# Optimization experiments

Measured on AMD Instinct MI355X. Metric: run time of the kernel, lower is better.

Reference implementation:

```python
import jax, jax.numpy as jnp
import numpy as np

N0, N1, N2 = 819200, 81920, 8192
E1, E2 = 819200, 81920
DIN, DH, DOUT = 128, 256, 128


def setup_inputs() -> dict:
    key = jax.random.key(0)
    ks = jax.random.split(key, 12)
    inp = {
        "x": jax.random.normal(ks[0], (N0, DIN), dtype=jnp.float32),
        "src1": jax.random.randint(ks[1], (E1,), 0, N0, dtype=jnp.int32),
        "dst1": jax.random.randint(ks[2], (E1,), 0, N1, dtype=jnp.int32),
        "src2": jax.random.randint(ks[3], (E2,), 0, N1, dtype=jnp.int32),
        "dst2": jax.random.randint(ks[4], (E2,), 0, N2, dtype=jnp.int32),
        "n1": N1,
        "n2": N2,
        # SAGEConv layer 1 params (lin_l has bias, lin_r no bias, PyG default)
        "w1l": jax.random.normal(ks[5], (DIN, DH), dtype=jnp.float32) / np.sqrt(DIN),
        "b1": jnp.zeros((DH,), dtype=jnp.float32),
        "w1r": jax.random.normal(ks[6], (DIN, DH), dtype=jnp.float32) / np.sqrt(DIN),
        # SAGEConv layer 2 params
        "w2l": jax.random.normal(ks[7], (DH, DOUT), dtype=jnp.float32) / np.sqrt(DH),
        "b2": jnp.zeros((DOUT,), dtype=jnp.float32),
        "w2r": jax.random.normal(ks[8], (DH, DOUT), dtype=jnp.float32) / np.sqrt(DH),
    }
    return inp


def _sage_conv(x_src, x_dst, src, dst, n_dst, wl, bl, wr):
    # mean aggregation of neighbor (source) features into destinations
    msg = x_src[src]                                            # [E, d]
    agg = jax.ops.segment_sum(msg, dst, num_segments=n_dst)     # [n_dst, d]
    cnt = jax.ops.segment_sum(jnp.ones((dst.shape[0],), msg.dtype), dst,
                              num_segments=n_dst)               # [n_dst]
    mean = agg / jnp.maximum(cnt, 1.0)[:, None]
    return mean @ wl + bl + x_dst @ wr


def reference(x, src1, dst1, src2, dst2, n1, n2, w1l, b1, w1r, w2l, b2, w2r):
    # layer 1 (eval mode: dropout is a no-op)
    h = _sage_conv(x, x[:n1], src1, dst1, n1, w1l, b1, w1r)     # [n1, DH]
    h = jax.nn.relu(h)
    # layer 2
    out = _sage_conv(h, h[:n2], src2, dst2, n2, w2l, b2, w2r)   # [n2, DOUT]
    return out
```

## Files before the change

kernel.cpp:

```cpp
#include <hip/hip_runtime.h>

constexpr int cN0 = 819200, cN1 = 81920, cN2 = 8192;
constexpr int cE1 = 819200, cE2 = 81920;
constexpr int cDIN = 128, cDH = 256, cDOUT = 128;
constexpr int cNOFF = cN1 + cN2;

typedef __attribute__((ext_vector_type(8))) short bf16x8;
typedef __attribute__((ext_vector_type(4))) float f32x4;
typedef __attribute__((ext_vector_type(8))) unsigned short u16x8;

__device__ __forceinline__ unsigned short f2bf(float f) {
    unsigned u = __builtin_bit_cast(unsigned, f);
    u += 0x7FFF + ((u >> 16) & 1);
    return (unsigned short)(u >> 16);
}
__device__ __forceinline__ float bf2f(unsigned short s) {
    unsigned u = ((unsigned)s) << 16;
    return __builtin_bit_cast(float, u);
}

#define GLOAD_LDS16(g, l) __builtin_amdgcn_global_load_lds(               \
    (const __attribute__((address_space(1))) void*)(g),                   \
    (__attribute__((address_space(3))) void*)(l), 16, 0, 0)

__global__ __launch_bounds__(256) void setup_k(
    int* __restrict__ offs,
    const float* __restrict__ w1l, const float* __restrict__ w1r,
    const float* __restrict__ w2l, const float* __restrict__ w2r,
    unsigned short* __restrict__ W1c, unsigned short* __restrict__ W2c,
    const float* __restrict__ x, unsigned short* __restrict__ xb)
{
    int id = blockIdx.x * 256 + threadIdx.x;
    if (id < cNOFF) { offs[id] = 0; return; }
    id -= cNOFF;
    if (id < 256 * 256) {
        int n = id >> 8, k = id & 255;
        float v = (k < 128) ? w1l[k * 256 + n] : w1r[(k - 128) * 256 + n];
        W1c[n * 256 + k] = f2bf(v);
        return;
    }
    id -= 256 * 256;
    if (id < 128 * 512) {
        int n = id >> 9, k = id & 511;
        float v = (k < 256) ? w2l[k * 128 + n] : w2r[(k - 256) * 128 + n];
        W2c[n * 512 + k] = f2bf(v);
        return;
    }
    id -= 128 * 512;
    {
        const float* p = x + (size_t)id * 8;
        float4 a = *reinterpret_cast<const float4*>(p);
        float4 b = *reinterpret_cast<const float4*>(p + 4);
        u16x8 o;
        o[0] = f2bf(a.x); o[1] = f2bf(a.y); o[2] = f2bf(a.z); o[3] = f2bf(a.w);
        o[4] = f2bf(b.x); o[5] = f2bf(b.y); o[6] = f2bf(b.z); o[7] = f2bf(b.w);
        reinterpret_cast<u16x8*>(xb)[id] = o;
    }
}

__global__ __launch_bounds__(256) void hist_k(
    const int* __restrict__ dst1, const int* __restrict__ dst2,
    int* __restrict__ offs)
{
    int e = blockIdx.x * 256 + threadIdx.x;
    if (e < cE1) atomicAdd(&offs[dst1[e]], 1);
    else {
        int e2 = e - cE1;
        if (e2 < cE2) atomicAdd(&offs[cN1 + dst2[e2]], 1);
    }
}

__global__ __launch_bounds__(1024) void partial_k(
    const int* __restrict__ a, int* __restrict__ part)
{
    const int tid = threadIdx.x, lane = tid & 63, wid = tid >> 6;
    int v = a[blockIdx.x * 1024 + tid];
    #pragma unroll
    for (int off = 32; off; off >>= 1) v += __shfl_xor(v, off);
    __shared__ int ws[16];
    if (lane == 0) ws[wid] = v;
    __syncthreads();
    if (tid == 0) {
        int s = 0;
        #pragma unroll
        for (int i = 0; i < 16; ++i) s += ws[i];
        part[blockIdx.x] = s;
    }
}

__global__ __launch_bounds__(128) void scanp_k(int* __restrict__ part)
{
    const int tid = threadIdx.x, lane = tid & 63, wid = tid >> 6;
    int v = (tid < 88) ? part[tid] : 0;
    int incl = v;
    #pragma unroll
    for (int off = 1; off < 64; off <<= 1) {
        int t = __shfl_up(incl, off, 64);
        if (lane >= off) incl += t;
    }
    __shared__ int w0;
    if (wid == 0 && lane == 63) w0 = incl;
    __syncthreads();
    int pre = wid ? w0 : 0;
    if (tid < 88) part[tid] = pre + incl - v;
}

__global__ __launch_bounds__(1024) void final_k(
    int* __restrict__ a, const int* __restrict__ part)
{
    const int tid = threadIdx.x, lane = tid & 63, wid = tid >> 6;
    const int g = blockIdx.x * 1024 + tid;
    int v = a[g];
    int incl = v;
    #pragma unroll
    for (int off = 1; off < 64; off <<= 1) {
        int t = __shfl_up(incl, off, 64);
        if (lane >= off) incl += t;
    }
    __shared__ int ws[16];
    if (lane == 63) ws[wid] = incl;
    __syncthreads();
    int pre = 0;
    #pragma unroll
    for (int i = 0; i < 16; ++i) if (i < wid) pre += ws[i];
    int r = part[blockIdx.x] + pre + incl - v;
    if (g >= cN1) r -= cE1;
    a[g] = r;
}

__global__ __launch_bounds__(256) void build_k(
    const int* __restrict__ src1, const int* __restrict__ dst1,
    const int* __restrict__ src2, const int* __restrict__ dst2,
    int* __restrict__ offs, int* __restrict__ eidx1, int* __restrict__ eidx2)
{
    int e = blockIdx.x * 256 + threadIdx.x;
    if (e < cE1) {
        int p = atomicAdd(&offs[dst1[e]], 1);
        eidx1[p] = src1[e];
    } else {
        int e2 = e - cE1;
        if (e2 < cE2) {
            int p = atomicAdd(&offs[cN1 + dst2[e2]], 1);
            eidx2[p] = src2[e2];
        }
    }
}

__global__ __launch_bounds__(256) void agg1_k(
    const float* __restrict__ x, const int* __restrict__ cursor,
    const int* __restrict__ eidx, unsigned short* __restrict__ mean1)
{
    const int row = blockIdx.x * 4 + (threadIdx.x >> 6);
    const int lane = threadIdx.x & 63;
    const int g = lane >> 4, li = lane & 15;
    const int start = row ? cursor[row - 1] : 0;
    const int end = cursor[row];
    float acc[8] = {};
    for (int e = start + g; e < end; e += 4) {
        const int s = eidx[e];
        const float4* p = reinterpret_cast<const float4*>(x + (size_t)s * cDIN + li * 8);
        float4 a = p[0], b = p[1];
        acc[0] += a.x; acc[1] += a.y; acc[2] += a.z; acc[3] += a.w;
        acc[4] += b.x; acc[5] += b.y; acc[6] += b.z; acc[7] += b.w;
    }
    #pragma unroll
    for (int i = 0; i < 8; ++i) {
        acc[i] += __shfl_xor(acc[i], 16);
        acc[i] += __shfl_xor(acc[i], 32);
    }
    if (g == 0) {
        const float inv = 1.0f / fmaxf((float)(end - start), 1.0f);
        u16x8 o;
        #pragma unroll
        for (int i = 0; i < 8; ++i) o[i] = f2bf(acc[i] * inv);
        *reinterpret_cast<u16x8*>(mean1 + (size_t)row * cDIN + li * 8) = o;
    }
}

__global__ __launch_bounds__(256) void agg2_k(
    const unsigned short* __restrict__ h, const int* __restrict__ cursor,
    const int* __restrict__ eidx, unsigned short* __restrict__ mean2)
{
    const int row = blockIdx.x * 4 + (threadIdx.x >> 6);
    const int lane = threadIdx.x & 63;
    const int g = lane >> 4, li = lane & 15;
    const int start = row ? cursor[row - 1] : 0;
    const int end = cursor[row];
    float acc[16] = {};
    for (int e = start + g; e < end; e += 4) {
        const int s = eidx[e];
        const u16x8* p = reinterpret_cast<const u16x8*>(h + (size_t)s * cDH + li * 16);
        u16x8 a = p[0], b = p[1];
        #pragma unroll
        for (int i = 0; i < 8; ++i) { acc[i] += bf2f(a[i]); acc[8 + i] += bf2f(b[i]); }
    }
    #pragma unroll
    for (int i = 0; i < 16; ++i) {
        acc[i] += __shfl_xor(acc[i], 16);
        acc[i] += __shfl_xor(acc[i], 32);
    }
    if (g == 0) {
        const float inv = 1.0f / fmaxf((float)(end - start), 1.0f);
        u16x8 o0, o1;
        #pragma unroll
        for (int i = 0; i < 8; ++i) { o0[i] = f2bf(acc[i] * inv); o1[i] = f2bf(acc[8 + i] * inv); }
        u16x8* q = reinterpret_cast<u16x8*>(mean2 + (size_t)row * cDH + li * 16);
        q[0] = o0; q[1] = o1;
    }
}

__global__ __launch_bounds__(256) void gemm1_k(
    const unsigned short* __restrict__ mean1,
    const unsigned short* __restrict__ xb,
    const unsigned short* __restrict__ W1c,
    const float* __restrict__ b1,
    unsigned short* __restrict__ h)
{
    __shared__ unsigned short As[128 * 32];
    __shared__ unsigned short Bs[128 * 32];

    const int tid = threadIdx.x;
    const int l = tid & 63, w = tid >> 6;
    const int q = l >> 4, r16 = l & 15;
    const int wr0 = (w >> 1) * 64, wc0 = (w & 1) * 64;
    const int n0 = blockIdx.x * 128, row0 = blockIdx.y * 128;

    const int srow = w * 32 + (l >> 2);
    const int skoff = (l & 3) * 8;

    const f32x4 zero = {0.f, 0.f, 0.f, 0.f};
    f32x4 acc[4][4];
    #pragma unroll
    for (int m = 0; m < 4; ++m)
        #pragma unroll
        for (int n = 0; n < 4; ++n) acc[m][n] = zero;

    for (int k0 = 0; k0 < 256; k0 += 32) {
        const unsigned short* Asrc = (k0 < 128) ? mean1 : xb;
        const int kk = k0 & 127;
        __syncthreads();
        #pragma unroll
        for (int j = 0; j < 2; ++j) {
            const int r = srow + j * 16;
            GLOAD_LDS16(Asrc + (size_t)(row0 + r) * 128 + kk + skoff,
                        As + (w * 2 + j) * 512);
            GLOAD_LDS16(W1c + (size_t)(n0 + r) * 256 + k0 + skoff,
                        Bs + (w * 2 + j) * 512);
        }
        __syncthreads();
        bf16x8 af[4], bg[4];
        #pragma unroll
        for (int m = 0; m < 4; ++m)
            af[m] = *reinterpret_cast<const bf16x8*>(As + (wr0 + 16 * m + r16) * 32 + q * 8);
        #pragma unroll
        for (int n = 0; n < 4; ++n)
            bg[n] = *reinterpret_cast<const bf16x8*>(Bs + (wc0 + 16 * n + r16) * 32 + q * 8);
        #pragma unroll
        for (int m = 0; m < 4; ++m)
            #pragma unroll
            for (int n = 0; n < 4; ++n)
                acc[m][n] = __builtin_amdgcn_mfma_f32_16x16x32_bf16(af[m], bg[n], acc[m][n], 0, 0, 0);
    }

    #pragma unroll
    for (int n = 0; n < 4; ++n) {
        const int col = n0 + wc0 + 16 * n + r16;
        const float bv = b1[col];
        #pragma unroll
        for (int m = 0; m < 4; ++m) {
            #pragma unroll
            for (int j = 0; j < 4; ++j) {
                const int row = row0 + wr0 + 16 * m + 4 * q + j;
                h[(size_t)row * cDH + col] = f2bf(fmaxf(acc[m][n][j] + bv, 0.f));
            }
        }
    }
}

__global__ __launch_bounds__(256) void gemm2_k(
    const unsigned short* __restrict__ mean2,
    const unsigned short* __restrict__ hd,
    const unsigned short* __restrict__ W2c,
    const float* __restrict__ b2, float* __restrict__ out)
{
    constexpr int K = 512, KL = 256, N = 128, TM = 64;
    constexpr int LD = 40;
    __shared__ unsigned short As[TM * LD];
    __shared__ unsigned short Bs[128 * LD];

    const int tid = threadIdx.x;
    const int l = tid & 63, w = tid >> 6;
    const int q = l >> 4, r16 = l & 15;
    const int wc0 = w * 32;
    const int row0 = blockIdx.y * TM;

    const f32x4 zero = {0.f, 0.f, 0.f, 0.f};
    f32x4 acc[4][2];
    #pragma unroll
    for (int m = 0; m < 4; ++m) { acc[m][0] = zero; acc[m][1] = zero; }

    for (int k0 = 0; k0 < K; k0 += 32) {
        const bool left = (k0 < KL);
        const unsigned short* Asrc = left ? mean2 : hd;
        const int kk = k0 & (KL - 1);
        __syncthreads();
        {
            int r = tid >> 2, o16 = tid & 3;
            bf16x8 av = *reinterpret_cast<const bf16x8*>(Asrc + (size_t)(row0 + r) * KL + kk + o16 * 8);
            *reinterpret_cast<bf16x8*>(As + r * LD + o16 * 8) = av;
        }
        #pragma unroll
        for (int c = 0; c < 2; ++c) {
            int z = tid + c * 256;
            int r = z >> 2, o16 = z & 3;
            bf16x8 bv = *reinterpret_cast<const bf16x8*>(W2c + (size_t)r * K + k0 + o16 * 8);
            *reinterpret_cast<bf16x8*>(Bs + r * LD + o16 * 8) = bv;
        }
        __syncthreads();
        bf16x8 af[4], bg[2];
        #pragma unroll
        for (int m = 0; m < 4; ++m)
            af[m] = *reinterpret_cast<const bf16x8*>(As + (16 * m + r16) * LD + q * 8);
        #pragma unroll
        for (int n = 0; n < 2; ++n)
            bg[n] = *reinterpret_cast<const bf16x8*>(Bs + (wc0 + 16 * n + r16) * LD + q * 8);
        #pragma unroll
        for (int m = 0; m < 4; ++m)
            #pragma unroll
            for (int n = 0; n < 2; ++n)
                acc[m][n] = __builtin_amdgcn_mfma_f32_16x16x32_bf16(af[m], bg[n], acc[m][n], 0, 0, 0);
    }

    #pragma unroll
    for (int n = 0; n < 2; ++n) {
        const int col = wc0 + 16 * n + r16;
        const float bv = b2[col];
        #pragma unroll
        for (int m = 0; m < 4; ++m) {
            #pragma unroll
            for (int j = 0; j < 4; ++j) {
                const int row = row0 + 16 * m + 4 * q + j;
                out[(size_t)row * N + col] = acc[m][n][j] + bv;
            }
        }
    }
}

extern "C" void kernel_launch(void* const* d_in, const int* in_sizes, int n_in,
                              void* d_out, int out_size, void* d_ws, size_t ws_size,
                              hipStream_t stream)
{
    const float* x    = (const float*)d_in[0];
    const int*   src1 = (const int*)d_in[1];
    const int*   dst1 = (const int*)d_in[2];
    const int*   src2 = (const int*)d_in[3];
    const int*   dst2 = (const int*)d_in[4];
    const float* w1l  = (const float*)d_in[7];
    const float* b1   = (const float*)d_in[8];
    const float* w1r  = (const float*)d_in[9];
    const float* w2l  = (const float*)d_in[10];
    const float* b2   = (const float*)d_in[11];
    const float* w2r  = (const float*)d_in[12];
    float* out = (float*)d_out;

    unsigned short* mean1 = (unsigned short*)d_ws;
    unsigned short* h     = mean1 + (size_t)cN1 * cDIN;
    unsigned short* mean2 = h + (size_t)cN1 * cDH;
    unsigned short* W1c   = mean2 + (size_t)cN2 * cDH;
    unsigned short* W2c   = W1c + 256 * 256;
    unsigned short* xb    = W2c + 128 * 512;
    int* offs  = (int*)(xb + (size_t)cN1 * cDIN);
    int* eidx1 = offs + cNOFF;
    int* eidx2 = eidx1 + cE1;
    int* part  = eidx2 + cE2;

    {
        int total = cNOFF + 256 * 256 + 128 * 512 + cN1 * cDIN / 8;
        setup_k<<<total / 256, 256, 0, stream>>>(offs, w1l, w1r, w2l, w2r,
                                                 W1c, W2c, x, xb);
    }
    hist_k<<<(cE1 + cE2) / 256, 256, 0, stream>>>(dst1, dst2, offs);
    partial_k<<<cNOFF / 1024, 1024, 0, stream>>>(offs, part);
    scanp_k<<<1, 128, 0, stream>>>(part);
    final_k<<<cNOFF / 1024, 1024, 0, stream>>>(offs, part);
    build_k<<<(cE1 + cE2) / 256, 256, 0, stream>>>(src1, dst1, src2, dst2, offs, eidx1, eidx2);

    agg1_k<<<cN1 / 4, 256, 0, stream>>>(x, offs, eidx1, mean1);
    gemm1_k<<<dim3(2, cN1 / 128), 256, 0, stream>>>(mean1, xb, W1c, b1, h);
    agg2_k<<<cN2 / 4, 256, 0, stream>>>(h, offs + cN1, eidx2, mean2);
    gemm2_k<<<dim3(1, cN2 / 64), 256, 0, stream>>>(mean2, h, W2c, b2, out);
}
```

Baseline: 246.1 us.

## Fuse histogram into setup, single-pass scan, and halve gemm2 row tile

Counter zeroing moves to a memset, and the destination histogram is folded into the setup kernel. The three-kernel scan (partial, scan of partials, final) becomes one kernel: block 0 spins on per-block flags to compute block prefixes and publishes them back. Together these cut the launch count and the dependency bubbles between the tiny preprocessing kernels. gemm2 uses 32-row tiles to double its block count for more parallelism on the small output, but each block now reloads the full weight matrix for half as many rows. The scan depends on all 88 blocks being co-resident, which holds on this GPU but is not guaranteed by the language.

```diff
diff --git a/kernel.cpp b/kernel.cpp
--- a/kernel.cpp
+++ b/kernel.cpp
@@ -2,8 +2,10 @@
 
 constexpr int cN0 = 819200, cN1 = 81920, cN2 = 8192;
 constexpr int cE1 = 819200, cE2 = 81920;
+constexpr int cEtot = cE1 + cE2;
 constexpr int cDIN = 128, cDH = 256, cDOUT = 128;
 constexpr int cNOFF = cN1 + cN2;
+constexpr int cSBLK = 88;
 
 typedef __attribute__((ext_vector_type(8))) short bf16x8;
 typedef __attribute__((ext_vector_type(4))) float f32x4;
@@ -23,16 +25,21 @@
     (const __attribute__((address_space(1))) void*)(g),                   \
     (__attribute__((address_space(3))) void*)(l), 16, 0, 0)
 
-__global__ __launch_bounds__(256) void setup_k(
+__global__ __launch_bounds__(256) void setup2_k(
     int* __restrict__ offs,
+    const int* __restrict__ dst1, const int* __restrict__ dst2,
     const float* __restrict__ w1l, const float* __restrict__ w1r,
     const float* __restrict__ w2l, const float* __restrict__ w2r,
     unsigned short* __restrict__ W1c, unsigned short* __restrict__ W2c,
     const float* __restrict__ x, unsigned short* __restrict__ xb)
 {
     int id = blockIdx.x * 256 + threadIdx.x;
-    if (id < cNOFF) { offs[id] = 0; return; }
-    id -= cNOFF;
+    if (id < cEtot) {
+        if (id < cE1) atomicAdd(&offs[dst1[id]], 1);
+        else atomicAdd(&offs[cN1 + dst2[id - cE1]], 1);
+        return;
+    }
+    id -= cEtot;
     if (id < 256 * 256) {
         int n = id >> 8, k = id & 255;
         float v = (k < 128) ? w1l[k * 256 + n] : w1r[(k - 128) * 256 + n];
@@ -58,72 +65,68 @@
     }
 }
 
-__global__ __launch_bounds__(256) void hist_k(
-    const int* __restrict__ dst1, const int* __restrict__ dst2,
-    int* __restrict__ offs)
-{
-    int e = blockIdx.x * 256 + threadIdx.x;
-    if (e < cE1) atomicAdd(&offs[dst1[e]], 1);
-    else {
-        int e2 = e - cE1;
-        if (e2 < cE2) atomicAdd(&offs[cN1 + dst2[e2]], 1);
-    }
-}
-
-__global__ __launch_bounds__(1024) void partial_k(
-    const int* __restrict__ a, int* __restrict__ part)
-{
-    const int tid = threadIdx.x, lane = tid & 63, wid = tid >> 6;
-    int v = a[blockIdx.x * 1024 + tid];
-    #pragma unroll
-    for (int off = 32; off; off >>= 1) v += __shfl_xor(v, off);
+__global__ __launch_bounds__(1024) void scan_lb_k(
+    int* __restrict__ a, unsigned* __restrict__ word)
+{
+    const int tid = threadIdx.x, bid = blockIdx.x;
+    const int lane = tid & 63, wid = tid >> 6;
+    const int g = bid * 1024 + tid;
     __shared__ int ws[16];
-    if (lane == 0) ws[wid] = v;
-    __syncthreads();
-    if (tid == 0) {
-        int s = 0;
-        #pragma unroll
-        for (int i = 0; i < 16; ++i) s += ws[i];
-        part[blockIdx.x] = s;
-    }
-}
-
-__global__ __launch_bounds__(128) void scanp_k(int* __restrict__ part)
-{
-    const int tid = threadIdx.x, lane = tid & 63, wid = tid >> 6;
-    int v = (tid < 88) ? part[tid] : 0;
+    __shared__ int aggs[cSBLK];
+    __shared__ int pex[cSBLK];
+    __shared__ int sh_excl;
+
+    int v = a[g];
     int incl = v;
     #pragma unroll
     for (int off = 1; off < 64; off <<= 1) {
         int t = __shfl_up(incl, off, 64);
         if (lane >= off) incl += t;
     }
-    __shared__ int w0;
-    if (wid == 0 && lane == 63) w0 = incl;
-    __syncthreads();
-    int pre = wid ? w0 : 0;
-    if (tid < 88) part[tid] = pre + incl - v;
-}
-
-__global__ __launch_bounds__(1024) void final_k(
-    int* __restrict__ a, const int* __restrict__ part)
-{
-    const int tid = threadIdx.x, lane = tid & 63, wid = tid >> 6;
-    const int g = blockIdx.x * 1024 + tid;
-    int v = a[g];
-    int incl = v;
-    #pragma unroll
-    for (int off = 1; off < 64; off <<= 1) {
-        int t = __shfl_up(incl, off, 64);
-        if (lane >= off) incl += t;
-    }
-    __shared__ int ws[16];
     if (lane == 63) ws[wid] = incl;
     __syncthreads();
-    int pre = 0;
-    #pragma unroll
-    for (int i = 0; i < 16; ++i) if (i < wid) pre += ws[i];
-    int r = part[blockIdx.x] + pre + incl - v;
+    int wpre = 0;
+    #pragma unroll
+    for (int w = 0; w < 15; ++w) if (w < wid) wpre += ws[w];
+    const int lexcl = wpre + incl - v;
+    if (tid == 0) {
+        int tot = 0;
+        #pragma unroll
+        for (int w = 0; w < 16; ++w) tot += ws[w];
+        __hip_atomic_store(&word[bid], ((unsigned)tot << 2) | 1u,
+                           __ATOMIC_RELEASE, __HIP_MEMORY_SCOPE_AGENT);
+    }
+
+    if (bid == 0) {
+        if (tid < cSBLK) {
+            unsigned wv;
+            do {
+                wv = __hip_atomic_load(&word[tid], __ATOMIC_ACQUIRE,
+                                       __HIP_MEMORY_SCOPE_AGENT);
+            } while ((wv & 3u) == 0u);
+            aggs[tid] = (int)(wv >> 2);
+        }
+        __syncthreads();
+        if (tid == 0) {
+            int run = 0;
+            for (int i = 0; i < cSBLK; ++i) { pex[i] = run; run += aggs[i]; }
+        }
+        __syncthreads();
+        if (tid < cSBLK)
+            __hip_atomic_store(&word[tid], ((unsigned)pex[tid] << 2) | 2u,
+                               __ATOMIC_RELEASE, __HIP_MEMORY_SCOPE_AGENT);
+    }
+
+    if (tid == 0) {
+        unsigned wv;
+        do {
+            wv = __hip_atomic_load(&word[bid], __ATOMIC_ACQUIRE,
+                                   __HIP_MEMORY_SCOPE_AGENT);
+        } while ((wv & 3u) != 2u);
+        sh_excl = (int)(wv >> 2);
+    }
+    __syncthreads();
+    int r = sh_excl + lexcl;
     if (g >= cN1) r -= cE1;
     a[g] = r;
 }
@@ -283,7 +286,7 @@
     const unsigned short* __restrict__ W2c,
     const float* __restrict__ b2, float* __restrict__ out)
 {
-    constexpr int K = 512, KL = 256, N = 128, TM = 64;
+    constexpr int K = 512, KL = 256, N = 128, TM = 32;
     constexpr int LD = 40;
     __shared__ unsigned short As[TM * LD];
     __shared__ unsigned short Bs[128 * LD];
@@ -295,16 +298,15 @@
     const int row0 = blockIdx.y * TM;
 
     const f32x4 zero = {0.f, 0.f, 0.f, 0.f};
-    f32x4 acc[4][2];
-    #pragma unroll
-    for (int m = 0; m < 4; ++m) { acc[m][0] = zero; acc[m][1] = zero; }
+    f32x4 acc[2][2];
+    acc[0][0] = zero; acc[0][1] = zero; acc[1][0] = zero; acc[1][1] = zero;
 
     for (int k0 = 0; k0 < K; k0 += 32) {
         const bool left = (k0 < KL);
         const unsigned short* Asrc = left ? mean2 : hd;
         const int kk = k0 & (KL - 1);
         __syncthreads();
-        {
+        if (tid < TM * 4) {
             int r = tid >> 2, o16 = tid & 3;
             bf16x8 av = *reinterpret_cast<const bf16x8*>(Asrc + (size_t)(row0 + r) * KL + kk + o16 * 8);
             *reinterpret_cast<bf16x8*>(As + r * LD + o16 * 8) = av;
@@ -317,15 +319,15 @@
             *reinterpret_cast<bf16x8*>(Bs + r * LD + o16 * 8) = bv;
         }
         __syncthreads();
-        bf16x8 af[4], bg[2];
-        #pragma unroll
-        for (int m = 0; m < 4; ++m)
+        bf16x8 af[2], bg[2];
+        #pragma unroll
+        for (int m = 0; m < 2; ++m)
             af[m] = *reinterpret_cast<const bf16x8*>(As + (16 * m + r16) * LD + q * 8);
         #pragma unroll
         for (int n = 0; n < 2; ++n)
             bg[n] = *reinterpret_cast<const bf16x8*>(Bs + (wc0 + 16 * n + r16) * LD + q * 8);
         #pragma unroll
-        for (int m = 0; m < 4; ++m)
+        for (int m = 0; m < 2; ++m)
             #pragma unroll
             for (int n = 0; n < 2; ++n)
                 acc[m][n] = __builtin_amdgcn_mfma_f32_16x16x32_bf16(af[m], bg[n], acc[m][n], 0, 0, 0);
@@ -336,7 +338,7 @@
         const int col = wc0 + 16 * n + r16;
         const float bv = b2[col];
         #pragma unroll
-        for (int m = 0; m < 4; ++m) {
+        for (int m = 0; m < 2; ++m) {
             #pragma unroll
             for (int j = 0; j < 4; ++j) {
                 const int row = row0 + 16 * m + 4 * q + j;
@@ -370,23 +372,21 @@
     unsigned short* W2c   = W1c + 256 * 256;
     unsigned short* xb    = W2c + 128 * 512;
     int* offs  = (int*)(xb + (size_t)cN1 * cDIN);
-    int* eidx1 = offs + cNOFF;
+    unsigned* word = (unsigned*)(offs + cNOFF);
+    int* eidx1 = (int*)(word + cSBLK);
     int* eidx2 = eidx1 + cE1;
-    int* part  = eidx2 + cE2;
-
+
+    hipMemsetAsync(offs, 0, (size_t)(cNOFF + cSBLK) * sizeof(int), stream);
     {
-        int total = cNOFF + 256 * 256 + 128 * 512 + cN1 * cDIN / 8;
-        setup_k<<<total / 256, 256, 0, stream>>>(offs, w1l, w1r, w2l, w2r,
-                                                 W1c, W2c, x, xb);
-    }
-    hist_k<<<(cE1 + cE2) / 256, 256, 0, stream>>>(dst1, dst2, offs);
-    partial_k<<<cNOFF / 1024, 1024, 0, stream>>>(offs, part);
-    scanp_k<<<1, 128, 0, stream>>>(part);
-    final_k<<<cNOFF / 1024, 1024, 0, stream>>>(offs, part);
+        int total = cEtot + 256 * 256 + 128 * 512 + cN1 * cDIN / 8;
+        setup2_k<<<total / 256, 256, 0, stream>>>(offs, dst1, dst2,
+                                                  w1l, w1r, w2l, w2r,
+                                                  W1c, W2c, x, xb);
+    }
+    scan_lb_k<<<cSBLK, 1024, 0, stream>>>(offs, word);
     build_k<<<(cE1 + cE2) / 256, 256, 0, stream>>>(src1, dst1, src2, dst2, offs, eidx1, eidx2);
-
     agg1_k<<<cN1 / 4, 256, 0, stream>>>(x, offs, eidx1, mean1);
     gemm1_k<<<dim3(2, cN1 / 128), 256, 0, stream>>>(mean1, xb, W1c, b1, h);
     agg2_k<<<cN2 / 4, 256, 0, stream>>>(h, offs + cN1, eidx2, mean2);
-    gemm2_k<<<dim3(1, cN2 / 64), 256, 0, stream>>>(mean2, h, W2c, b2, out);
-}
+    gemm2_k<<<dim3(1, cN2 / 32), 256, 0, stream>>>(mean2, h, W2c, b2, out);
+}
```

Result: no change. 242.7 us (-1.4%).
